# Kernel optimization log

Hardware: AMD Instinct MI355X
Metric: run time of the kernel (lower is better)

The kernel has to match this reference:

```python
import jax, jax.numpy as jnp
import numpy as np

B, IN = 8192, 8000
C, S, O = 16, 500, 64          # num_chunks, chunk_size, fc_repr_dim
F = C * O                       # fc_0_out_feat = 1024
E, D, T = 8, 512, 2            # num_experts, fc_task_dim, num_tasks
NC = (32, 2)                    # num_classes per task
EPS = 1e-5


def _bn(h, g, b, axis):
    # training-mode BatchNorm1d: biased variance over the batch axis
    m = h.mean(axis=axis, keepdims=True)
    v = h.var(axis=axis, keepdims=True)
    return (h - m) * jax.lax.rsqrt(v + EPS) * g + b


def _swish(x):
    return x * jax.nn.sigmoid(x)


def setup_inputs() -> dict:
    key = jax.random.key(0)
    ks = jax.random.split(key, 10)
    s = 0.02
    return {
        "x": jax.random.normal(ks[0], (B, IN), dtype=jnp.float32),
        "w0": jax.random.normal(ks[1], (C, O, S), dtype=jnp.float32) * s,
        "b0": jnp.zeros((F,), jnp.float32),
        "bn0_g": jnp.ones((F,), jnp.float32),
        "bn0_b": jnp.zeros((F,), jnp.float32),
        "gate_w": jax.random.normal(ks[2], (T, F, E), dtype=jnp.float32) * s,
        "gate_b": jnp.zeros((T, E), jnp.float32),
        "exp_w": jax.random.normal(ks[3], (E, F, D), dtype=jnp.float32) * s,
        "exp_bn_g": jnp.ones((E, D), jnp.float32),
        "exp_bn_b": jnp.zeros((E, D), jnp.float32),
        "task_w": jax.random.normal(ks[4], (T, D, D), dtype=jnp.float32) * s,
        "task_bn_g": jnp.ones((T, D), jnp.float32),
        "task_bn_b": jnp.zeros((T, D), jnp.float32),
        "fin_w_a": jax.random.normal(ks[5], (D, NC[0]), dtype=jnp.float32) * s,
        "fin_b_a": jnp.zeros((NC[0],), jnp.float32),
        "fin_w_b": jax.random.normal(ks[6], (D, NC[1]), dtype=jnp.float32) * s,
        "fin_b_b": jnp.zeros((NC[1],), jnp.float32),
    }


def reference(x, w0, b0, bn0_g, bn0_b, gate_w, gate_b, exp_w, exp_bn_g,
              exp_bn_b, task_w, task_bn_g, task_bn_b, fin_w_a, fin_b_a,
              fin_w_b, fin_b_b):
    b = x.shape[0]
    # SplitLinear: block-diagonal linear over C chunks of size S -> O each
    h0 = jnp.einsum('bcs,cos->bco', x.reshape(b, C, S), w0).reshape(b, F) + b0
    h0 = _swish(_bn(h0, bn0_g, bn0_b, axis=0))                  # [B, F]
    # per-task gates with softmax over experts
    gates = jax.nn.softmax(
        jnp.einsum('bf,tfe->tbe', h0, gate_w) + gate_b[:, None, :], axis=-1)
    # expert branches: Linear(no bias) + BN + Swish, vectorized over experts
    eh = jnp.einsum('bf,efd->bed', h0, exp_w)                   # [B, E, D]
    eh = _swish(_bn(eh, exp_bn_g, exp_bn_b, axis=0))
    # gate-weighted sum over experts, per task
    mix = jnp.einsum('tbe,bed->tbd', gates, eh)                 # [T, B, D]
    # task branches: Linear(no bias) + BN + Swish
    th = jnp.einsum('tbd,tdk->tbk', mix, task_w)
    th = _swish(_bn(th, task_bn_g[:, None, :], task_bn_b[:, None, :], axis=1))
    out_a = th[0] @ fin_w_a + fin_b_a                           # [B, 32]
    out_b = th[1] @ fin_w_b + fin_b_b                           # [B, 2]
    return jnp.concatenate([out_a, out_b], axis=1)             # [B, 34]
```

## Files before the change

### kernel.cpp

```cpp
#include <hip/hip_runtime.h>
#include <math.h>

#define B_ 8192
#define IN_ 8000
#define C_ 16
#define S_ 500
#define O_ 64
#define F_ 1024
#define E_ 8
#define D_ 512
#define T_ 2
#define OUTW 34
#define EPS_ 1e-5f

typedef __attribute__((ext_vector_type(8))) short bf16x8;
typedef __attribute__((ext_vector_type(4))) float f32x4;

__device__ __forceinline__ float swishf(float x) {
    return x / (1.0f + __expf(-x));
}

__device__ __forceinline__ unsigned short f2bf(float f) {
    union { float f; unsigned u; } c;
    c.f = f;
    unsigned r = c.u + 0x7fffu + ((c.u >> 16) & 1u);
    return (unsigned short)(r >> 16);
}
__device__ __forceinline__ float bf2f(unsigned short b) {
    union { unsigned u; float f; } c;
    c.u = ((unsigned)b) << 16;
    return c.f;
}

__device__ __forceinline__ void gld16(const void* g, void* l) {
    __builtin_amdgcn_global_load_lds(
        (const __attribute__((address_space(1))) void*)g,
        (__attribute__((address_space(3))) void*)l, 16, 0, 0);
}

__global__ __launch_bounds__(256) void k_split(const float* __restrict__ x,
                                               const float* __restrict__ w0,
                                               const float* __restrict__ b0,
                                               float* __restrict__ h0,
                                               float* __restrict__ psum,
                                               float* __restrict__ psq) {
    const int KT = 20;
    __shared__ __align__(16) float xs[KT][132];
    __shared__ __align__(16) float wsh[KT][68];
    int tid = threadIdx.x;
    int tx = tid & 15, ty = tid >> 4;
    int c = blockIdx.y;
    int brow0 = blockIdx.x * 128;
    const float* xp = x + (size_t)brow0 * IN_ + c * S_;
    const float* wp = w0 + (size_t)c * O_ * S_;
    float acc[8][4];
#pragma unroll
    for (int r = 0; r < 8; r++)
#pragma unroll
        for (int j = 0; j < 4; j++) acc[r][j] = 0.f;

    for (int k0 = 0; k0 < S_; k0 += KT) {
#pragma unroll
        for (int i = 0; i < 10; i++) {
            int li = tid + i * 256;
            int bi = li / KT, k = li % KT;
            xs[k][bi] = xp[(size_t)bi * IN_ + k0 + k];
        }
#pragma unroll
        for (int i = 0; i < 5; i++) {
            int li = tid + i * 256;
            int oi = li / KT, k = li % KT;
            wsh[k][oi] = wp[oi * S_ + k0 + k];
        }
        __syncthreads();
#pragma unroll
        for (int k = 0; k < KT; k++) {
            float a[8], wv[4];
#pragma unroll
            for (int r = 0; r < 8; r++) a[r] = xs[k][ty * 8 + r];
#pragma unroll
            for (int j = 0; j < 4; j++) wv[j] = wsh[k][tx * 4 + j];
#pragma unroll
            for (int r = 0; r < 8; r++)
#pragma unroll
                for (int j = 0; j < 4; j++) acc[r][j] += a[r] * wv[j];
        }
        __syncthreads();
    }

    float s[4] = {0.f, 0.f, 0.f, 0.f}, q[4] = {0.f, 0.f, 0.f, 0.f};
    int ocol0 = c * O_ + tx * 4;
    float bb[4];
#pragma unroll
    for (int j = 0; j < 4; j++) bb[j] = b0[ocol0 + j];
#pragma unroll
    for (int r = 0; r < 8; r++) {
        float4 v;
        float vv[4];
#pragma unroll
        for (int j = 0; j < 4; j++) {
            vv[j] = acc[r][j] + bb[j];
            s[j] += vv[j];
            q[j] += vv[j] * vv[j];
        }
        v.x = vv[0]; v.y = vv[1]; v.z = vv[2]; v.w = vv[3];
        *(float4*)(h0 + (size_t)(brow0 + ty * 8 + r) * F_ + ocol0) = v;
    }
#pragma unroll
    for (int j = 0; j < 4; j++) {
        s[j] += __shfl_down(s[j], 32, 64); s[j] += __shfl_down(s[j], 16, 64);
        q[j] += __shfl_down(q[j], 32, 64); q[j] += __shfl_down(q[j], 16, 64);
    }
    float* red = &xs[0][0];
    int wv_ = tid >> 6, lane = tid & 63;
    if (lane < 16) {
#pragma unroll
        for (int j = 0; j < 4; j++) {
            red[(wv_ * 16 + lane) * 4 + j] = s[j];
            red[256 + (wv_ * 16 + lane) * 4 + j] = q[j];
        }
    }
    __syncthreads();
    if (tid < 64) {
        int txc = tid >> 2, j = tid & 3;
        float ss = 0.f, qq = 0.f;
#pragma unroll
        for (int w = 0; w < 4; w++) {
            ss += red[(w * 16 + txc) * 4 + j];
            qq += red[256 + (w * 16 + txc) * 4 + j];
        }
        size_t idx = (size_t)blockIdx.x * F_ + c * O_ + tid;
        psum[idx] = ss; psq[idx] = qq;
    }
}

__global__ __launch_bounds__(64) void k_stats_b(const float* __restrict__ psum,
                                                const float* __restrict__ psq,
                                                int N, int YS,
                                                const float* __restrict__ g,
                                                const float* __restrict__ beta,
                                                unsigned long long gslab,
                                                float* __restrict__ scale,
                                                float* __restrict__ shift,
                                                unsigned long long oslab) {
    int n = blockIdx.x * 64 + threadIdx.x;
    int z = blockIdx.z;
    float s = 0.f, q = 0.f;
    for (int y = 0; y < YS; y++) {
        size_t idx = ((size_t)(z * YS + y)) * N + n;
        s += psum[idx]; q += psq[idx];
    }
    float mean = s * (1.0f / B_);
    float var = q * (1.0f / B_) - mean * mean;
    float sc = g[z * gslab + n] * rsqrtf(var + EPS_);
    scale[z * oslab + n] = sc;
    shift[z * oslab + n] = beta[z * gslab + n] - mean * sc;
}

__global__ __launch_bounds__(256) void k_wt(const float* __restrict__ in,
                                            unsigned short* __restrict__ out,
                                            int K, int N) {
    __shared__ float t[32][33];
    int k0 = blockIdx.x * 32, n0 = blockIdx.y * 32, z = blockIdx.z;
    const float* ip = in + (size_t)z * K * N;
    unsigned short* op = out + (size_t)z * N * K;
    int tn = threadIdx.x & 31, tk = threadIdx.x >> 5;
#pragma unroll
    for (int p = 0; p < 4; p++) {
        int k = tk + p * 8;
        t[k][tn] = ip[(size_t)(k0 + k) * N + n0 + tn];
    }
    __syncthreads();
    int tk2 = threadIdx.x & 31, tn2 = threadIdx.x >> 5;
#pragma unroll
    for (int p = 0; p < 4; p++) {
        int n = tn2 + p * 8;
        op[(size_t)(n0 + n) * K + k0 + tk2] = f2bf(t[tk2][n]);
    }
}

__global__ __launch_bounds__(256) void k_bnswish_gates(const float* __restrict__ h0,
                                                       const float* __restrict__ scale,
                                                       const float* __restrict__ shift,
                                                       const float* __restrict__ gate_w,
                                                       const float* __restrict__ gate_b,
                                                       unsigned short* __restrict__ h0bf,
                                                       float* __restrict__ gates) {
    int b = blockIdx.x, tid = threadIdx.x;
    float part[16];
#pragma unroll
    for (int i = 0; i < 16; i++) part[i] = 0.f;
    const float* row = h0 + (size_t)b * F_;
    unsigned short* ob = h0bf + (size_t)b * F_;
#pragma unroll
    for (int it = 0; it < 4; it++) {
        int f = tid + it * 256;
        float v = row[f];
        float hv = scale[f] * v + shift[f];
        float sw = swishf(hv);
        ob[f] = f2bf(sw);
        const float* gw0 = gate_w + (size_t)f * E_;
        const float* gw1 = gate_w + (size_t)(F_ * E_) + (size_t)f * E_;
#pragma unroll
        for (int e = 0; e < E_; e++) part[e] += sw * gw0[e];
#pragma unroll
        for (int e = 0; e < E_; e++) part[8 + e] += sw * gw1[e];
    }
#pragma unroll
    for (int i = 0; i < 16; i++) {
        float v = part[i];
        for (int off = 32; off > 0; off >>= 1) v += __shfl_down(v, off, 64);
        part[i] = v;
    }
    __shared__ float red[4][16];
    __shared__ float gfin[16];
    int wave = tid >> 6, lane = tid & 63;
    if (lane == 0) {
#pragma unroll
        for (int i = 0; i < 16; i++) red[wave][i] = part[i];
    }
    __syncthreads();
    if (tid < 16) {
        float v = red[0][tid] + red[1][tid] + red[2][tid] + red[3][tid];
        int t = tid >> 3, e = tid & 7;
        gfin[tid] = v + gate_b[t * E_ + e];
    }
    __syncthreads();
    if (tid < 2) {
        float mx = -1e30f;
#pragma unroll
        for (int e = 0; e < 8; e++) mx = fmaxf(mx, gfin[tid * 8 + e]);
        float ex[8], sum = 0.f;
#pragma unroll
        for (int e = 0; e < 8; e++) { ex[e] = __expf(gfin[tid * 8 + e] - mx); sum += ex[e]; }
        float inv = 1.0f / sum;
#pragma unroll
        for (int e = 0; e < 8; e++)
            gates[(size_t)tid * (B_ * E_) + (size_t)b * E_ + e] = ex[e] * inv;
    }
}

__global__ __launch_bounds__(256) void k_gemm_bf16(const unsigned short* __restrict__ A,
                                                   unsigned long long aslab,
                                                   const unsigned short* __restrict__ Wt,
                                                   unsigned long long wslab,
                                                   unsigned short* __restrict__ C,
                                                   unsigned long long cslab, int K,
                                                   float* __restrict__ psum,
                                                   float* __restrict__ psq) {
    __shared__ __align__(16) unsigned short As[128 * 32];
    __shared__ __align__(16) unsigned short Ws[128 * 32];
    int z = blockIdx.z;
    A  += (size_t)z * aslab;
    Wt += (size_t)z * wslab;
    C  += (size_t)z * cslab;
    const int N = gridDim.y * 128;
    int row0 = blockIdx.x * 128, col0 = blockIdx.y * 128;
    int tid = threadIdx.x;
    int w = tid >> 6, lane = tid & 63;
    int l15 = lane & 15, quad = lane >> 4;

    const unsigned short* ga0 = A  + (size_t)(row0 + w * 32 + (lane >> 2)) * K + (lane & 3) * 8;
    const unsigned short* ga1 = ga0 + 16 * (size_t)K;
    const unsigned short* gw0 = Wt + (size_t)(col0 + w * 32 + (lane >> 2)) * K + (lane & 3) * 8;
    const unsigned short* gw1 = gw0 + 16 * (size_t)K;
    unsigned short* la0 = As + (w * 32) * 32;
    unsigned short* la1 = As + (w * 32 + 16) * 32;
    unsigned short* lw0 = Ws + (w * 32) * 32;
    unsigned short* lw1 = Ws + (w * 32 + 16) * 32;

    int wm = (w & 1) * 64, wn = (w >> 1) * 64;
    const unsigned short* Afr = As + (size_t)(wm + l15) * 32 + quad * 8;
    const unsigned short* Wfr = Ws + (size_t)(wn + l15) * 32 + quad * 8;

    f32x4 acc[4][4] = {};

    for (int k0 = 0; k0 < K; k0 += 32) {
        gld16(ga0 + k0, la0);
        gld16(ga1 + k0, la1);
        gld16(gw0 + k0, lw0);
        gld16(gw1 + k0, lw1);
        __syncthreads();
        bf16x8 af[4], wf[4];
#pragma unroll
        for (int i = 0; i < 4; i++) af[i] = *(const bf16x8*)(Afr + i * 16 * 32);
#pragma unroll
        for (int j = 0; j < 4; j++) wf[j] = *(const bf16x8*)(Wfr + j * 16 * 32);
#pragma unroll
        for (int i = 0; i < 4; i++)
#pragma unroll
            for (int j = 0; j < 4; j++)
                acc[i][j] = __builtin_amdgcn_mfma_f32_16x16x32_bf16(af[i], wf[j], acc[i][j], 0, 0, 0);
        __syncthreads();
    }

#pragma unroll
    for (int i = 0; i < 4; i++) {
        int r = row0 + wm + i * 16 + quad * 4;
#pragma unroll
        for (int j = 0; j < 4; j++) {
            int cc = col0 + wn + j * 16 + l15;
            unsigned short* cp = C + (size_t)r * N + cc;
#pragma unroll
            for (int reg = 0; reg < 4; reg++)
                cp[(size_t)reg * N] = f2bf(acc[i][j][reg]);
        }
    }

    float* red = (float*)As;
    float sj[4], qj[4];
#pragma unroll
    for (int j = 0; j < 4; j++) {
        float s = 0.f, q = 0.f;
#pragma unroll
        for (int i = 0; i < 4; i++)
#pragma unroll
            for (int reg = 0; reg < 4; reg++) {
                float v = acc[i][j][reg];
                s += v; q += v * v;
            }
        s += __shfl_down(s, 32, 64); s += __shfl_down(s, 16, 64);
        q += __shfl_down(q, 32, 64); q += __shfl_down(q, 16, 64);
        sj[j] = s; qj[j] = q;
    }
    if (lane < 16) {
#pragma unroll
        for (int j = 0; j < 4; j++) {
            int cib = wn + j * 16 + lane;
            red[cib * 2 + (w & 1)] = sj[j];
            red[256 + cib * 2 + (w & 1)] = qj[j];
        }
    }
    __syncthreads();
    if (tid < 128) {
        float s = red[tid * 2] + red[tid * 2 + 1];
        float q = red[256 + tid * 2] + red[256 + tid * 2 + 1];
        size_t row = (size_t)z * gridDim.x + blockIdx.x;
        psum[row * N + col0 + tid] = s;
        psq[row * N + col0 + tid] = q;
    }
}

__global__ __launch_bounds__(512) void k_mix(const unsigned short* __restrict__ eh,
                                             const float* __restrict__ scale,
                                             const float* __restrict__ shift,
                                             const float* __restrict__ gates,
                                             unsigned short* __restrict__ mix) {
    int b = blockIdx.x, d = threadIdx.x;
    __shared__ float gl[2][8];
    if (threadIdx.x < 16)
        gl[threadIdx.x >> 3][threadIdx.x & 7] =
            gates[(size_t)(threadIdx.x >> 3) * (B_ * E_) + (size_t)b * E_ + (threadIdx.x & 7)];
    __syncthreads();
    float a0 = 0.f, a1 = 0.f;
#pragma unroll
    for (int e = 0; e < E_; e++) {
        int n = e * D_ + d;
        float v = bf2f(eh[(size_t)b * (E_ * D_) + n]);
        float hv = scale[n] * v + shift[n];
        float sw = swishf(hv);
        a0 += gl[0][e] * sw;
        a1 += gl[1][e] * sw;
    }
    mix[(size_t)b * D_ + d] = f2bf(a0);
    mix[(size_t)(B_ * D_) + (size_t)b * D_ + d] = f2bf(a1);
}

__global__ __launch_bounds__(64) void k_final(const unsigned short* __restrict__ th,
                                              const float* __restrict__ scale,
                                              const float* __restrict__ shift,
                                              const float* __restrict__ fwa,
                                              const float* __restrict__ fba,
                                              const float* __restrict__ fwb,
                                              const float* __restrict__ fbb,
                                              float* __restrict__ out) {
    __shared__ float t0[D_], t1[D_];
    int b = blockIdx.x, tid = threadIdx.x;
    for (int i = tid; i < D_; i += 64) {
        float v0 = bf2f(th[(size_t)b * D_ + i]);
        t0[i] = swishf(scale[i] * v0 + shift[i]);
        float v1 = bf2f(th[(size_t)(B_ * D_) + (size_t)b * D_ + i]);
        t1[i] = swishf(scale[D_ + i] * v1 + shift[D_ + i]);
    }
    __syncthreads();
    if (tid < 32) {
        float acc = fba[tid];
        for (int d = 0; d < D_; d++) acc += t0[d] * fwa[d * 32 + tid];
        out[(size_t)b * OUTW + tid] = acc;
    } else if (tid < 34) {
        int j = tid - 32;
        float acc = fbb[j];
        for (int d = 0; d < D_; d++) acc += t1[d] * fwb[d * 2 + j];
        out[(size_t)b * OUTW + tid] = acc;
    }
}

extern "C" void kernel_launch(void* const* d_in, const int* in_sizes, int n_in,
                              void* d_out, int out_size, void* d_ws, size_t ws_size,
                              hipStream_t stream) {
    const float* x        = (const float*)d_in[0];
    const float* w0       = (const float*)d_in[1];
    const float* b0       = (const float*)d_in[2];
    const float* bn0_g    = (const float*)d_in[3];
    const float* bn0_b    = (const float*)d_in[4];
    const float* gate_w   = (const float*)d_in[5];
    const float* gate_b   = (const float*)d_in[6];
    const float* exp_w    = (const float*)d_in[7];
    const float* exp_bn_g = (const float*)d_in[8];
    const float* exp_bn_b = (const float*)d_in[9];
    const float* task_w   = (const float*)d_in[10];
    const float* task_bn_g= (const float*)d_in[11];
    const float* task_bn_b= (const float*)d_in[12];
    const float* fwa      = (const float*)d_in[13];
    const float* fba      = (const float*)d_in[14];
    const float* fwb      = (const float*)d_in[15];
    const float* fbb      = (const float*)d_in[16];
    float* out = (float*)d_out;

    float* ws = (float*)d_ws;
    unsigned short* ehbf = (unsigned short*)ws;
    float* h0            = ws + 16777216;
    unsigned short* thbf = ehbf;
    unsigned short* mixbf= (unsigned short*)h0;
    unsigned short* h0bf = (unsigned short*)(ws + 25165824);
    unsigned short* wtE  = (unsigned short*)(ws + 29360128);
    unsigned short* twt  = (unsigned short*)(ws + 31457280);
    float* gates = ws + 31719424;
    float* sc0   = ws + 31850496;
    float* sh0   = sc0 + 1024;
    float* scE   = sh0 + 1024;
    float* shE   = scE + 4096;
    float* scT   = shE + 4096;
    float* shT   = scT + 1024;
    float* psum  = shT + 1024;
    float* psq   = psum + 262144;

    k_wt<<<dim3(32, 16, 8), 256, 0, stream>>>(exp_w, wtE, F_, D_);
    k_wt<<<dim3(16, 16, 2), 256, 0, stream>>>(task_w, twt, D_, D_);
    k_split<<<dim3(64, 16), 256, 0, stream>>>(x, w0, b0, h0, psum, psq);
    k_stats_b<<<dim3(16, 1, 1), 64, 0, stream>>>(psum, psq, F_, 64, bn0_g, bn0_b, 0ull, sc0, sh0, 0ull);
    k_bnswish_gates<<<dim3(B_), 256, 0, stream>>>(h0, sc0, sh0, gate_w, gate_b, h0bf, gates);
    k_gemm_bf16<<<dim3(64, 32, 1), 256, 0, stream>>>(h0bf, 0ull, wtE, 0ull, ehbf, 0ull, F_, psum, psq);
    k_stats_b<<<dim3(64, 1, 1), 64, 0, stream>>>(psum, psq, E_ * D_, 64, exp_bn_g, exp_bn_b, 0ull, scE, shE, 0ull);
    k_mix<<<dim3(B_), 512, 0, stream>>>(ehbf, scE, shE, gates, mixbf);
    k_gemm_bf16<<<dim3(64, 4, 2), 256, 0, stream>>>(mixbf, (unsigned long long)(B_ * D_),
                                                    twt, (unsigned long long)(D_ * D_),
                                                    thbf, (unsigned long long)(B_ * D_), D_,
                                                    psum, psq);
    k_stats_b<<<dim3(8, 1, 2), 64, 0, stream>>>(psum, psq, D_, 64, task_bn_g, task_bn_b, 512ull, scT, shT, 512ull);
    k_final<<<dim3(B_), 64, 0, stream>>>(thbf, scT, shT, fwa, fba, fwb, fbb, out);
}
```

Measured before the change: 750.1 us.

## Use bf16 MFMA for split linear, store h0 as bf16, batch mix/final rows

The block-diagonal split linear moves from scalar FP32 FMA to bf16 MFMA 16x16x32. Inputs are converted to bf16 while staging into LDS, and K is zero-padded from 500 to 512. The pre-BN activation h0 is now written as bf16, which halves that intermediate's traffic and shrinks the workspace layout. k_mix is vectorised (4 elements per thread, two rows per block, BN scale/shift cached in LDS), and k_final handles 8 rows per block with a split reduction for the 2-class head. The trade-off is lower precision on the first layer's inputs and on h0 before batch-norm statistics are applied.

Result: faster. 689.6 us (-8.1%).

```diff
diff --git a/kernel.cpp b/kernel.cpp
--- a/kernel.cpp
+++ b/kernel.cpp
@@ -41,95 +41,99 @@
 __global__ __launch_bounds__(256) void k_split(const float* __restrict__ x,
                                                const float* __restrict__ w0,
                                                const float* __restrict__ b0,
-                                               float* __restrict__ h0,
+                                               unsigned short* __restrict__ h0raw,
                                                float* __restrict__ psum,
                                                float* __restrict__ psq) {
-    const int KT = 20;
-    __shared__ __align__(16) float xs[KT][132];
-    __shared__ __align__(16) float wsh[KT][68];
+    __shared__ __align__(16) unsigned short As[128 * 72];
+    __shared__ __align__(16) unsigned short Bs[64 * 72];
     int tid = threadIdx.x;
-    int tx = tid & 15, ty = tid >> 4;
     int c = blockIdx.y;
     int brow0 = blockIdx.x * 128;
     const float* xp = x + (size_t)brow0 * IN_ + c * S_;
     const float* wp = w0 + (size_t)c * O_ * S_;
-    float acc[8][4];
-#pragma unroll
-    for (int r = 0; r < 8; r++)
-#pragma unroll
-        for (int j = 0; j < 4; j++) acc[r][j] = 0.f;
-
-    for (int k0 = 0; k0 < S_; k0 += KT) {
-#pragma unroll
-        for (int i = 0; i < 10; i++) {
+
+    int w = tid >> 6, lane = tid & 63;
+    int l15 = lane & 15, quad = lane >> 4;
+    int wm = w * 32;
+
+    f32x4 acc[2][4] = {};
+
+    for (int k0 = 0; k0 < 512; k0 += 64) {
+#pragma unroll
+        for (int i = 0; i < 8; i++) {
             int li = tid + i * 256;
-            int bi = li / KT, k = li % KT;
-            xs[k][bi] = xp[(size_t)bi * IN_ + k0 + k];
-        }
-#pragma unroll
-        for (int i = 0; i < 5; i++) {
+            int row = li >> 4, c4 = li & 15;
+            int gk = k0 + c4 * 4;
+            float4 v = make_float4(0.f, 0.f, 0.f, 0.f);
+            if (gk + 3 < S_) v = *(const float4*)(xp + (size_t)row * IN_ + gk);
+            unsigned short u[4] = { f2bf(v.x), f2bf(v.y), f2bf(v.z), f2bf(v.w) };
+            *(ushort4*)&As[row * 72 + c4 * 4] = *(ushort4*)u;
+        }
+#pragma unroll
+        for (int i = 0; i < 4; i++) {
             int li = tid + i * 256;
-            int oi = li / KT, k = li % KT;
-            wsh[k][oi] = wp[oi * S_ + k0 + k];
+            int row = li >> 4, c4 = li & 15;
+            int gk = k0 + c4 * 4;
+            float4 v = make_float4(0.f, 0.f, 0.f, 0.f);
+            if (gk + 3 < S_) v = *(const float4*)(wp + (size_t)row * S_ + gk);
+            unsigned short u[4] = { f2bf(v.x), f2bf(v.y), f2bf(v.z), f2bf(v.w) };
+            *(ushort4*)&Bs[row * 72 + c4 * 4] = *(ushort4*)u;
         }
         __syncthreads();
 #pragma unroll
-        for (int k = 0; k < KT; k++) {
-            float a[8], wv[4];
-#pragma unroll
-            for (int r = 0; r < 8; r++) a[r] = xs[k][ty * 8 + r];
-#pragma unroll
-            for (int j = 0; j < 4; j++) wv[j] = wsh[k][tx * 4 + j];
-#pragma unroll
-            for (int r = 0; r < 8; r++)
-#pragma unroll
-                for (int j = 0; j < 4; j++) acc[r][j] += a[r] * wv[j];
+        for (int kk = 0; kk < 64; kk += 32) {
+            bf16x8 af[2], wf[4];
+#pragma unroll
+            for (int i = 0; i < 2; i++)
+                af[i] = *(const bf16x8*)&As[(wm + i * 16 + l15) * 72 + kk + quad * 8];
+#pragma unroll
+            for (int j = 0; j < 4; j++)
+                wf[j] = *(const bf16x8*)&Bs[(j * 16 + l15) * 72 + kk + quad * 8];
+#pragma unroll
+            for (int i = 0; i < 2; i++)
+#pragma unroll
+                for (int j = 0; j < 4; j++)
+                    acc[i][j] = __builtin_amdgcn_mfma_f32_16x16x32_bf16(af[i], wf[j], acc[i][j], 0, 0, 0);
         }
         __syncthreads();
     }
 
-    float s[4] = {0.f, 0.f, 0.f, 0.f}, q[4] = {0.f, 0.f, 0.f, 0.f};
-    int ocol0 = c * O_ + tx * 4;
-    float bb[4];
-#pragma unroll
-    for (int j = 0; j < 4; j++) bb[j] = b0[ocol0 + j];
-#pragma unroll
-    for (int r = 0; r < 8; r++) {
-        float4 v;
-        float vv[4];
+    int colbase = c * O_;
+    float sj[4], qj[4];
+#pragma unroll
+    for (int j = 0; j < 4; j++) {
+        int col = j * 16 + l15;
+        float bb = b0[colbase + col];
+        float s = 0.f, q = 0.f;
+#pragma unroll
+        for (int i = 0; i < 2; i++) {
+#pragma unroll
+            for (int reg = 0; reg < 4; reg++) {
+                float v = acc[i][j][reg] + bb;
+                int rl = wm + i * 16 + quad * 4 + reg;
+                h0raw[(size_t)(brow0 + rl) * F_ + colbase + col] = f2bf(v);
+                s += v; q += v * v;
+            }
+        }
+        s += __shfl_down(s, 32, 64); s += __shfl_down(s, 16, 64);
+        q += __shfl_down(q, 32, 64); q += __shfl_down(q, 16, 64);
+        sj[j] = s; qj[j] = q;
+    }
+    __syncthreads();
+    float* red = (float*)As;
+    if (lane < 16) {
 #pragma unroll
         for (int j = 0; j < 4; j++) {
-            vv[j] = acc[r][j] + bb[j];
-            s[j] += vv[j];
-            q[j] += vv[j] * vv[j];
-        }
-        v.x = vv[0]; v.y = vv[1]; v.z = vv[2]; v.w = vv[3];
-        *(float4*)(h0 + (size_t)(brow0 + ty * 8 + r) * F_ + ocol0) = v;
-    }
-#pragma unroll
-    for (int j = 0; j < 4; j++) {
-        s[j] += __shfl_down(s[j], 32, 64); s[j] += __shfl_down(s[j], 16, 64);
-        q[j] += __shfl_down(q[j], 32, 64); q[j] += __shfl_down(q[j], 16, 64);
-    }
-    float* red = &xs[0][0];
-    int wv_ = tid >> 6, lane = tid & 63;
-    if (lane < 16) {
-#pragma unroll
-        for (int j = 0; j < 4; j++) {
-            red[(wv_ * 16 + lane) * 4 + j] = s[j];
-            red[256 + (wv_ * 16 + lane) * 4 + j] = q[j];
+            int col = j * 16 + l15;
+            red[col * 4 + w] = sj[j];
+            red[256 + col * 4 + w] = qj[j];
         }
     }
     __syncthreads();
     if (tid < 64) {
-        int txc = tid >> 2, j = tid & 3;
-        float ss = 0.f, qq = 0.f;
-#pragma unroll
-        for (int w = 0; w < 4; w++) {
-            ss += red[(w * 16 + txc) * 4 + j];
-            qq += red[256 + (w * 16 + txc) * 4 + j];
-        }
-        size_t idx = (size_t)blockIdx.x * F_ + c * O_ + tid;
+        float ss = red[tid * 4] + red[tid * 4 + 1] + red[tid * 4 + 2] + red[tid * 4 + 3];
+        float qq = red[256 + tid * 4] + red[256 + tid * 4 + 1] + red[256 + tid * 4 + 2] + red[256 + tid * 4 + 3];
+        size_t idx = (size_t)blockIdx.x * F_ + colbase + tid;
         psum[idx] = ss; psq[idx] = qq;
     }
 }
@@ -179,7 +183,7 @@
     }
 }
 
-__global__ __launch_bounds__(256) void k_bnswish_gates(const float* __restrict__ h0,
+__global__ __launch_bounds__(256) void k_bnswish_gates(const unsigned short* __restrict__ h0,
                                                        const float* __restrict__ scale,
                                                        const float* __restrict__ shift,
                                                        const float* __restrict__ gate_w,
@@ -190,12 +194,12 @@
     float part[16];
 #pragma unroll
     for (int i = 0; i < 16; i++) part[i] = 0.f;
-    const float* row = h0 + (size_t)b * F_;
+    const unsigned short* row = h0 + (size_t)b * F_;
     unsigned short* ob = h0bf + (size_t)b * F_;
 #pragma unroll
     for (int it = 0; it < 4; it++) {
         int f = tid + it * 256;
-        float v = row[f];
+        float v = bf2f(row[f]);
         float hv = scale[f] * v + shift[f];
         float sw = swishf(hv);
         ob[f] = f2bf(sw);
@@ -341,57 +345,97 @@
     }
 }
 
-__global__ __launch_bounds__(512) void k_mix(const unsigned short* __restrict__ eh,
+__global__ __launch_bounds__(256) void k_mix(const unsigned short* __restrict__ eh,
                                              const float* __restrict__ scale,
                                              const float* __restrict__ shift,
                                              const float* __restrict__ gates,
                                              unsigned short* __restrict__ mix) {
-    int b = blockIdx.x, d = threadIdx.x;
-    __shared__ float gl[2][8];
-    if (threadIdx.x < 16)
-        gl[threadIdx.x >> 3][threadIdx.x & 7] =
-            gates[(size_t)(threadIdx.x >> 3) * (B_ * E_) + (size_t)b * E_ + (threadIdx.x & 7)];
-    __syncthreads();
-    float a0 = 0.f, a1 = 0.f;
+    __shared__ float scl[E_ * D_], shl[E_ * D_];
+    __shared__ float gl[2][2][8];
+    int tid = threadIdx.x;
+#pragma unroll
+    for (int i = 0; i < 4; i++) {
+        int li = tid + i * 256;
+        ((float4*)scl)[li] = ((const float4*)scale)[li];
+        ((float4*)shl)[li] = ((const float4*)shift)[li];
+    }
+    if (tid < 32) {
+        int sub = tid >> 4, t = (tid >> 3) & 1, e = tid & 7;
+        gl[sub][t][e] = gates[(size_t)t * (B_ * E_) + (size_t)(blockIdx.x * 2 + sub) * E_ + e];
+    }
+    __syncthreads();
+    int sub = tid >> 7;
+    int b = blockIdx.x * 2 + sub;
+    int d0 = (tid & 127) * 4;
+    float a0[4] = {0.f, 0.f, 0.f, 0.f}, a1[4] = {0.f, 0.f, 0.f, 0.f};
 #pragma unroll
     for (int e = 0; e < E_; e++) {
-        int n = e * D_ + d;
-        float v = bf2f(eh[(size_t)b * (E_ * D_) + n]);
-        float hv = scale[n] * v + shift[n];
-        float sw = swishf(hv);
-        a0 += gl[0][e] * sw;
-        a1 += gl[1][e] * sw;
-    }
-    mix[(size_t)b * D_ + d] = f2bf(a0);
-    mix[(size_t)(B_ * D_) + (size_t)b * D_ + d] = f2bf(a1);
-}
-
-__global__ __launch_bounds__(64) void k_final(const unsigned short* __restrict__ th,
-                                              const float* __restrict__ scale,
-                                              const float* __restrict__ shift,
-                                              const float* __restrict__ fwa,
-                                              const float* __restrict__ fba,
-                                              const float* __restrict__ fwb,
-                                              const float* __restrict__ fbb,
-                                              float* __restrict__ out) {
-    __shared__ float t0[D_], t1[D_];
-    int b = blockIdx.x, tid = threadIdx.x;
-    for (int i = tid; i < D_; i += 64) {
-        float v0 = bf2f(th[(size_t)b * D_ + i]);
-        t0[i] = swishf(scale[i] * v0 + shift[i]);
-        float v1 = bf2f(th[(size_t)(B_ * D_) + (size_t)b * D_ + i]);
-        t1[i] = swishf(scale[D_ + i] * v1 + shift[D_ + i]);
-    }
-    __syncthreads();
-    if (tid < 32) {
-        float acc = fba[tid];
-        for (int d = 0; d < D_; d++) acc += t0[d] * fwa[d * 32 + tid];
-        out[(size_t)b * OUTW + tid] = acc;
-    } else if (tid < 34) {
-        int j = tid - 32;
-        float acc = fbb[j];
-        for (int d = 0; d < D_; d++) acc += t1[d] * fwb[d * 2 + j];
-        out[(size_t)b * OUTW + tid] = acc;
+        ushort4 u = *(const ushort4*)&eh[(size_t)b * (E_ * D_) + e * D_ + d0];
+        float4 sc4 = *(const float4*)&scl[e * D_ + d0];
+        float4 sh4 = *(const float4*)&shl[e * D_ + d0];
+        float g0 = gl[sub][0][e], g1 = gl[sub][1][e];
+        unsigned short uu[4] = { u.x, u.y, u.z, u.w };
+        float scv[4] = { sc4.x, sc4.y, sc4.z, sc4.w };
+        float shv[4] = { sh4.x, sh4.y, sh4.z, sh4.w };
+#pragma unroll
+        for (int l = 0; l < 4; l++) {
+            float sw = swishf(scv[l] * bf2f(uu[l]) + shv[l]);
+            a0[l] += g0 * sw;
+            a1[l] += g1 * sw;
+        }
+    }
+    unsigned short o0[4], o1[4];
+#pragma unroll
+    for (int l = 0; l < 4; l++) { o0[l] = f2bf(a0[l]); o1[l] = f2bf(a1[l]); }
+    *(ushort4*)&mix[(size_t)b * D_ + d0] = *(ushort4*)o0;
+    *(ushort4*)&mix[(size_t)(B_ * D_) + (size_t)b * D_ + d0] = *(ushort4*)o1;
+}
+
+__global__ __launch_bounds__(256) void k_final(const unsigned short* __restrict__ th,
+                                               const float* __restrict__ scale,
+                                               const float* __restrict__ shift,
+                                               const float* __restrict__ fwa,
+                                               const float* __restrict__ fba,
+                                               const float* __restrict__ fwb,
+                                               const float* __restrict__ fbb,
+                                               float* __restrict__ out) {
+    __shared__ float t0[8][D_], t1[8][D_];
+    __shared__ float pb[64];
+    int tid = threadIdx.x;
+    int b0 = blockIdx.x * 8;
+#pragma unroll
+    for (int t = 0; t < 2; t++) {
+#pragma unroll
+        for (int i = 0; i < 4; i++) {
+            int li = tid + i * 256;
+            int row = li >> 7, d = (li & 127) * 4;
+            ushort4 u = *(const ushort4*)&th[((size_t)t * B_ + b0 + row) * D_ + d];
+            unsigned short uu[4] = { u.x, u.y, u.z, u.w };
+            float* dst = t ? &t1[row][d] : &t0[row][d];
+#pragma unroll
+            for (int l = 0; l < 4; l++)
+                dst[l] = swishf(scale[t * D_ + d + l] * bf2f(uu[l]) + shift[t * D_ + d + l]);
+        }
+    }
+    __syncthreads();
+    {
+        int row = tid >> 5, col = tid & 31;
+        float acc = fba[col];
+        for (int d = 0; d < D_; d++) acc += t0[row][d] * fwa[d * 32 + col];
+        out[(size_t)(b0 + row) * OUTW + col] = acc;
+    }
+    if (tid < 64) {
+        int row = tid >> 3, colb = (tid >> 2) & 1, part = tid & 3;
+        float a = 0.f;
+        for (int d = part * 128; d < part * 128 + 128; d++) a += t1[row][d] * fwb[d * 2 + colb];
+        pb[tid] = a;
+    }
+    __syncthreads();
+    if (tid < 16) {
+        int row = tid >> 1, colb = tid & 1;
+        int base = row * 8 + colb * 4;
+        float a = fbb[colb] + pb[base] + pb[base + 1] + pb[base + 2] + pb[base + 3];
+        out[(size_t)(b0 + row) * OUTW + 32 + colb] = a;
     }
 }
 
@@ -418,15 +462,15 @@
     float* out = (float*)d_out;
 
     float* ws = (float*)d_ws;
-    unsigned short* ehbf = (unsigned short*)ws;
-    float* h0            = ws + 16777216;
-    unsigned short* thbf = ehbf;
-    unsigned short* mixbf= (unsigned short*)h0;
-    unsigned short* h0bf = (unsigned short*)(ws + 25165824);
-    unsigned short* wtE  = (unsigned short*)(ws + 29360128);
-    unsigned short* twt  = (unsigned short*)(ws + 31457280);
-    float* gates = ws + 31719424;
-    float* sc0   = ws + 31850496;
+    unsigned short* ehbf  = (unsigned short*)ws;
+    unsigned short* h0raw = (unsigned short*)(ws + 16777216);
+    unsigned short* thbf  = ehbf;
+    unsigned short* mixbf = h0raw;
+    unsigned short* h0bf  = (unsigned short*)(ws + 20971520);
+    unsigned short* wtE   = (unsigned short*)(ws + 25165824);
+    unsigned short* twt   = (unsigned short*)(ws + 27262976);
+    float* gates = ws + 27525120;
+    float* sc0   = ws + 27656192;
     float* sh0   = sc0 + 1024;
     float* scE   = sh0 + 1024;
     float* shE   = scE + 4096;
@@ -437,16 +481,16 @@
 
     k_wt<<<dim3(32, 16, 8), 256, 0, stream>>>(exp_w, wtE, F_, D_);
     k_wt<<<dim3(16, 16, 2), 256, 0, stream>>>(task_w, twt, D_, D_);
-    k_split<<<dim3(64, 16), 256, 0, stream>>>(x, w0, b0, h0, psum, psq);
+    k_split<<<dim3(64, 16), 256, 0, stream>>>(x, w0, b0, h0raw, psum, psq);
     k_stats_b<<<dim3(16, 1, 1), 64, 0, stream>>>(psum, psq, F_, 64, bn0_g, bn0_b, 0ull, sc0, sh0, 0ull);
-    k_bnswish_gates<<<dim3(B_), 256, 0, stream>>>(h0, sc0, sh0, gate_w, gate_b, h0bf, gates);
+    k_bnswish_gates<<<dim3(B_), 256, 0, stream>>>(h0raw, sc0, sh0, gate_w, gate_b, h0bf, gates);
     k_gemm_bf16<<<dim3(64, 32, 1), 256, 0, stream>>>(h0bf, 0ull, wtE, 0ull, ehbf, 0ull, F_, psum, psq);
     k_stats_b<<<dim3(64, 1, 1), 64, 0, stream>>>(psum, psq, E_ * D_, 64, exp_bn_g, exp_bn_b, 0ull, scE, shE, 0ull);
-    k_mix<<<dim3(B_), 512, 0, stream>>>(ehbf, scE, shE, gates, mixbf);
+    k_mix<<<dim3(B_ / 2), 256, 0, stream>>>(ehbf, scE, shE, gates, mixbf);
     k_gemm_bf16<<<dim3(64, 4, 2), 256, 0, stream>>>(mixbf, (unsigned long long)(B_ * D_),
                                                     twt, (unsigned long long)(D_ * D_),
                                                     thbf, (unsigned long long)(B_ * D_), D_,
                                                     psum, psq);
     k_stats_b<<<dim3(8, 1, 2), 64, 0, stream>>>(psum, psq, D_, 64, task_bn_g, task_bn_b, 512ull, scT, shT, 512ull);
-    k_final<<<dim3(B_), 64, 0, stream>>>(thbf, scT, shT, fwa, fba, fwb, fbb, out);
-}
+    k_final<<<dim3(B_ / 8), 256, 0, stream>>>(thbf, scT, shT, fwa, fba, fwb, fbb, out);
+}
```
